# Optimization experiments

Measured on AMD Instinct MI355X. Metric: run time of the kernel, lower is better.

The kernel has to match this reference:

```python
import jax, jax.numpy as jnp
import numpy as np

B, S, E, H = 4, 1024, 1024, 16
D = E // H          # head_dim = 64
ROT = 32            # rotary dims (first ROT channels of each head)


def _rope(x, freqs):
    # x: [B, H, S, D]; freqs: [1, 1, S, ROT]
    r = freqs.shape[-1]
    xl, xr = x[..., :r], x[..., r:]
    half = r // 2
    rot = jnp.concatenate([-xl[..., half:], xl[..., :half]], axis=-1)  # rotate_half
    xl = xl * jnp.cos(freqs) + rot * jnp.sin(freqs)
    return jnp.concatenate([xl, xr], axis=-1)


def setup_inputs() -> dict:
    key = jax.random.key(0)
    ks = jax.random.split(key, 7)
    std = 0.02
    return {
        "hidden_states": jax.random.normal(ks[0], (B, S, E), jnp.float32),
        "rotary_pos_emb": jax.random.normal(ks[1], (1, S, ROT), jnp.float32),
        "q_w": jax.random.normal(ks[2], (E, E), jnp.float32) * std,
        "k_w": jax.random.normal(ks[3], (E, E), jnp.float32) * std,
        "v_w": jax.random.normal(ks[4], (E, E), jnp.float32) * std,
        "o_w": jax.random.normal(ks[5], (E, E), jnp.float32) * std,
        "o_b": jnp.zeros((E,), jnp.float32),
    }


def reference(hidden_states, rotary_pos_emb, q_w, k_w, v_w, o_w, o_b):
    bsz, tgt_len, embed_dim = hidden_states.shape
    scale = D ** -0.5

    def shape(t):  # [B, S, E] -> [B, H, S, D]
        return t.reshape(bsz, tgt_len, H, D).transpose(0, 2, 1, 3)

    q = shape(hidden_states @ q_w.T * scale)
    k = shape(hidden_states @ k_w.T)
    v = shape(hidden_states @ v_w.T)

    freqs = rotary_pos_emb[:, None, :, :]  # [1, 1, S, ROT]
    q = _rope(q, freqs)
    k = _rope(k, freqs)
    v = _rope(v, freqs)

    attn = jnp.einsum("bhqd,bhkd->bhqk", q, k)
    causal = jnp.tril(jnp.ones((tgt_len, tgt_len), bool))
    attn = jnp.where(causal, attn, jnp.finfo(attn.dtype).min)
    attn = jax.nn.softmax(attn, axis=-1)

    out = jnp.einsum("bhqk,bhkd->bhqd", attn, v)
    out = out.transpose(0, 2, 1, 3).reshape(bsz, tgt_len, embed_dim)
    return out @ o_w.T + o_b
```

## Files before the change

### kernel.cpp

```cpp
#include <hip/hip_runtime.h>
#include <hip/hip_bf16.h>

typedef __bf16 bf16;
typedef __attribute__((ext_vector_type(2))) __bf16 bf16x2;
typedef __attribute__((ext_vector_type(4))) __bf16 bf16x4;
typedef __attribute__((ext_vector_type(8))) __bf16 bf16x8;
typedef __attribute__((ext_vector_type(4))) float f32x4;

#define NB 4
#define NS 1024
#define NE 1024
#define NH 16
#define ND 64
#define NROT 32
#define NM (NB*NS)

__device__ __forceinline__ void gload_lds16(const bf16* g, void* l) {
  __builtin_amdgcn_global_load_lds(
      (const __attribute__((address_space(1))) unsigned int*)g,
      (__attribute__((address_space(3))) unsigned int*)l,
      16, 0, 0);
}

struct PrepArgs {
  const float* w0; const float* w1; const float* w2; const float* w3;
  bf16* b0; bf16* b1; bf16* b2; bf16* b3;
  const float* hs; bf16* hb;
  const float* rot; float* ct; float* st;
};
__global__ void k_prep(PrepArgs a) {
  const int y = blockIdx.y;
  const int i = blockIdx.x * 256 + threadIdx.x;
  if (y < 4) {
    const float* s = (y == 0) ? a.w0 : (y == 1) ? a.w1 : (y == 2) ? a.w2 : a.w3;
    bf16* d = (y == 0) ? a.b0 : (y == 1) ? a.b1 : (y == 2) ? a.b2 : a.b3;
    float4 v = reinterpret_cast<const float4*>(s)[i];
    bf16x4 o = { (bf16)v.x, (bf16)v.y, (bf16)v.z, (bf16)v.w };
    *reinterpret_cast<bf16x4*>(d + (size_t)i * 4) = o;
  } else if (y < 8) {
    size_t off = (size_t)(y - 4) * (NM * NE / 16);
    float4 v = reinterpret_cast<const float4*>(a.hs)[off + i];
    bf16x4 o = { (bf16)v.x, (bf16)v.y, (bf16)v.z, (bf16)v.w };
    *reinterpret_cast<bf16x4*>(a.hb + (off + i) * 4) = o;
  } else {
    if (i < NS * NROT) {
      float v = a.rot[i];
      a.ct[i] = cosf(v);
      a.st[i] = sinf(v);
    }
  }
}

__global__ __launch_bounds__(512) void k_proj(
    const bf16* __restrict__ A, const bf16* __restrict__ Wq, const bf16* __restrict__ Wk,
    const bf16* __restrict__ Wv, bf16* __restrict__ Oq, bf16* __restrict__ Ok,
    bf16* __restrict__ vt, const float* __restrict__ ct, const float* __restrict__ st)
{
  __shared__ bf16 lA[2 * 128 * 64];
  __shared__ bf16 lW[3][2 * 128 * 64];
  const int m0 = blockIdx.x * 128, n0 = blockIdx.y * 128;
  const int tid = threadIdx.x;
  const int wave = tid >> 6, lane = tid & 63;
  const int wm = wave >> 2, wn = wave & 3;
  const int fr = lane & 15, kg = lane >> 4;
  const int lrow8 = lane >> 3, lslot = lane & 7;

  auto stageG = [&](int kt, int c, int g) {
    const bf16* src = (g == 0) ? A : (g == 1) ? Wq : (g == 2) ? Wk : Wv;
    bf16* dst = (g == 0) ? lA : lW[g - 1];
    const int base0 = (g == 0) ? m0 : n0;
#pragma unroll
    for (int i = 0; i < 2; ++i) {
      int chunk = wave * 2 + i;
      int row = (chunk << 3) + lrow8;
      int slot = lslot ^ (row & 7);
      gload_lds16(src + (size_t)(base0 + row) * NE + kt + slot * 8,
                  (char*)dst + c * 16384 + chunk * 1024);
    }
  };

#pragma unroll
  for (int g = 0; g < 4; ++g) stageG(0, 0, g);
  asm volatile("s_waitcnt vmcnt(0)\n\ts_barrier" ::: "memory");

  constexpr int NT = NE / 64;
  f32x4 aq[4][2] = {}, ak[4][2] = {}, av[2][4] = {};
  bf16x8 bq[2][2], bk[2][2], bv[2][2];

  for (int t = 0; t < NT; ++t) {
    const int c = t & 1;
    const bf16* cA = lA + c * 8192;
    const bf16* cQ = lW[0] + c * 8192;
    const bf16* cK = lW[1] + c * 8192;
    const bf16* cV = lW[2] + c * 8192;

#pragma unroll
    for (int q = 0; q < 4; ++q) {
      if (t + 1 < NT) {
        if (q == 0) { stageG((t + 1) * 64, c ^ 1, 0); stageG((t + 1) * 64, c ^ 1, 1); }
        else if (q < 3) stageG((t + 1) * 64, c ^ 1, q + 1);
      }

      if (q == 0) {
        if (t > 0) {
          if (t + 1 < NT)
            asm volatile("s_waitcnt vmcnt(4)\n\ts_barrier" ::: "memory");
          else
            asm volatile("s_waitcnt vmcnt(0)\n\ts_barrier" ::: "memory");
        }
#pragma unroll
        for (int j = 0; j < 2; ++j) {
          int rb = wn * 32 + j * 16 + fr;
          int off0 = rb * 64 + (((kg + 0) ^ (rb & 7)) << 3);
          int off1 = rb * 64 + (((kg + 4) ^ (rb & 7)) << 3);
          bq[j][0] = *reinterpret_cast<const bf16x8*>(cQ + off0);
          bq[j][1] = *reinterpret_cast<const bf16x8*>(cQ + off1);
          bk[j][0] = *reinterpret_cast<const bf16x8*>(cK + off0);
          bk[j][1] = *reinterpret_cast<const bf16x8*>(cK + off1);
          bv[j][0] = *reinterpret_cast<const bf16x8*>(cV + off0);
          bv[j][1] = *reinterpret_cast<const bf16x8*>(cV + off1);
        }
      }

      bf16x8 af[2];
      {
        int ra = wm * 64 + q * 16 + fr;
        af[0] = *reinterpret_cast<const bf16x8*>(cA + ra * 64 + (((kg + 0) ^ (ra & 7)) << 3));
        af[1] = *reinterpret_cast<const bf16x8*>(cA + ra * 64 + (((kg + 4) ^ (ra & 7)) << 3));
      }

      __builtin_amdgcn_sched_barrier(0);
      __builtin_amdgcn_s_setprio(1);
#pragma unroll
      for (int kk = 0; kk < 2; ++kk)
#pragma unroll
        for (int j = 0; j < 2; ++j) {
          aq[q][j] = __builtin_amdgcn_mfma_f32_16x16x32_bf16(af[kk], bq[j][kk], aq[q][j], 0, 0, 0);
          ak[q][j] = __builtin_amdgcn_mfma_f32_16x16x32_bf16(af[kk], bk[j][kk], ak[q][j], 0, 0, 0);
          av[j][q] = __builtin_amdgcn_mfma_f32_16x16x32_bf16(bv[j][kk], af[kk], av[j][q], 0, 0, 0);
        }
      __builtin_amdgcn_s_setprio(0);
      __builtin_amdgcn_sched_barrier(0);
    }

    asm volatile("s_waitcnt lgkmcnt(0)\n\ts_barrier" ::: "memory");
  }

  const int nb = n0 + wn * 32;
  const bool ropeHalf = ((nb & 63) == 0);
  const float qscale = 0.125f * 1.44269504f;

#pragma unroll
  for (int p = 0; p < 4; ++p)
#pragma unroll
    for (int r = 0; r < 4; ++r) {
      int gm = m0 + wm * 64 + p * 16 + kg * 4 + r;
      int s = gm & (NS - 1);
      size_t rb = (size_t)gm * NE + nb;
      float q0v = aq[p][0][r] * qscale, q1v = aq[p][1][r] * qscale;
      float k0v = ak[p][0][r],          k1v = ak[p][1][r];
      if (ropeHalf) {
        float c0 = ct[s * NROT + fr],      sn0 = st[s * NROT + fr];
        float c1 = ct[s * NROT + 16 + fr], sn1 = st[s * NROT + 16 + fr];
        Oq[rb + fr]      = (bf16)(q0v * c0 - q1v * sn0);
        Oq[rb + 16 + fr] = (bf16)(q1v * c1 + q0v * sn1);
        Ok[rb + fr]      = (bf16)(k0v * c0 - k1v * sn0);
        Ok[rb + 16 + fr] = (bf16)(k1v * c1 + k0v * sn1);
      } else {
        Oq[rb + fr]      = (bf16)q0v;
        Oq[rb + 16 + fr] = (bf16)q1v;
        Ok[rb + fr]      = (bf16)k0v;
        Ok[rb + 16 + fr] = (bf16)k1v;
      }
    }

  {
    const int b = m0 >> 10;
    const int h = nb >> 6;
    const int eb = nb & 63;
    bf16* vtb = vt + ((size_t)(b * 16 + h)) * ND * NS;
#pragma unroll
    for (int i = 0; i < 4; ++i) {
      int sl = (m0 & (NS - 1)) + wm * 64 + i * 16 + fr;
#pragma unroll
      for (int r = 0; r < 4; ++r) {
        int dbase = kg * 4 + r;
        float x0 = av[0][i][r];
        float x1 = av[1][i][r];
        if (eb == 0) {
          float c0 = ct[sl * NROT + dbase],      sn0 = st[sl * NROT + dbase];
          float c1 = ct[sl * NROT + 16 + dbase], sn1 = st[sl * NROT + 16 + dbase];
          vtb[(size_t)(dbase)      * NS + sl] = (bf16)(x0 * c0 - x1 * sn0);
          vtb[(size_t)(16 + dbase) * NS + sl] = (bf16)(x1 * c1 + x0 * sn1);
        } else {
          vtb[(size_t)(32 + dbase) * NS + sl] = (bf16)x0;
          vtb[(size_t)(48 + dbase) * NS + sl] = (bf16)x1;
        }
      }
    }
  }
}

__global__ __launch_bounds__(256) void k_gemm_o(
    const bf16* __restrict__ A, const bf16* __restrict__ W, float* __restrict__ Og,
    const float* __restrict__ bias)
{
  __shared__ bf16 lA[64 * 64];
  __shared__ bf16 lB[128 * 64];
  const int m0 = blockIdx.x * 64, n0 = blockIdx.y * 128;
  const int tid = threadIdx.x;
  const int wave = tid >> 6, lane = tid & 63;
  const int wm = wave >> 1, wn = wave & 1;
  const int fr = lane & 15, kg = lane >> 4;
  const int lrow8 = lane >> 3, lslot = lane & 7;

  f32x4 acc[2][4] = {};

  for (int kt = 0; kt < NE; kt += 64) {
#pragma unroll
    for (int i = 0; i < 2; ++i) {
      int chunk = i * 4 + wave;
      int row = (chunk << 3) + lrow8;
      int slot = lslot ^ (row & 7);
      gload_lds16(A + (size_t)(m0 + row) * NE + kt + slot * 8, (char*)lA + chunk * 1024);
    }
#pragma unroll
    for (int i = 0; i < 4; ++i) {
      int chunk = i * 4 + wave;
      int row = (chunk << 3) + lrow8;
      int slot = lslot ^ (row & 7);
      gload_lds16(W + (size_t)(n0 + row) * NE + kt + slot * 8, (char*)lB + chunk * 1024);
    }
    __syncthreads();
#pragma unroll
    for (int kk = 0; kk < 2; ++kk) {
      bf16x8 af[2], bfr[4];
#pragma unroll
      for (int i = 0; i < 2; ++i) {
        int ra = wm * 32 + i * 16 + fr;
        af[i] = *reinterpret_cast<const bf16x8*>(lA + ra * 64 + (((kg + 4 * kk) ^ (ra & 7)) << 3));
      }
#pragma unroll
      for (int j = 0; j < 4; ++j) {
        int rb = wn * 64 + j * 16 + fr;
        bfr[j] = *reinterpret_cast<const bf16x8*>(lB + rb * 64 + (((kg + 4 * kk) ^ (rb & 7)) << 3));
      }
#pragma unroll
      for (int i = 0; i < 2; ++i)
#pragma unroll
        for (int j = 0; j < 4; ++j)
          acc[i][j] = __builtin_amdgcn_mfma_f32_16x16x32_bf16(af[i], bfr[j], acc[i][j], 0, 0, 0);
    }
    __syncthreads();
  }

#pragma unroll
  for (int i = 0; i < 2; ++i)
#pragma unroll
    for (int j = 0; j < 4; ++j) {
      int gc = n0 + wn * 64 + j * 16 + fr;
      float bv = bias[gc];
#pragma unroll
      for (int r = 0; r < 4; ++r) {
        int gm = m0 + wm * 32 + i * 16 + kg * 4 + r;
        Og[(size_t)gm * NE + gc] = acc[i][j][r] + bv;
      }
    }
}

__global__ __launch_bounds__(256) void k_attn(
    const bf16* __restrict__ Q, const bf16* __restrict__ K,
    const bf16* __restrict__ VT, bf16* __restrict__ O)
{
  __shared__ bf16 lK[2][64 * 64];
  __shared__ bf16 lVT[2][64 * 64];
  __shared__ bf16 lP[4][16 * 68];
  const int tid = threadIdx.x;
  const int wave = tid >> 6, lane = tid & 63;
  const int fr = lane & 15, kg = lane >> 4;

  const int qt = 15 - (blockIdx.y >> 3);
  const int bh = blockIdx.x | ((blockIdx.y & 7) << 3);
  const int b = bh >> 4, h = bh & 15;
  const int nt = qt + 1;
  const bf16* Qb  = Q + (size_t)b * NS * NE + h * 64;
  const bf16* Kb  = K + (size_t)b * NS * NE + h * 64;
  const bf16* VTb = VT + (size_t)bh * ND * NS;
  bf16* Ob = O + (size_t)b * NS * NE + h * 64;

  const int qrow0 = qt * 64 + wave * 16;

  bf16x8 qf[2];
#pragma unroll
  for (int kk = 0; kk < 2; ++kk)
    qf[kk] = *reinterpret_cast<const bf16x8*>(
        Qb + (size_t)(qrow0 + fr) * NE + kk * 32 + kg * 8);

  const int srow = lane >> 3;
  const int sslot = (lane & 7) ^ srow;
  const int r0 = wave * 8 + srow;
  const int r1 = (wave + 4) * 8 + srow;
  const bf16* kA0 = Kb + (size_t)r0 * NE + sslot * 8;
  const bf16* kA1 = Kb + (size_t)r1 * NE + sslot * 8;
  const bf16* vA0 = VTb + (size_t)r0 * NS + sslot * 8;
  const bf16* vA1 = VTb + (size_t)r1 * NS + sslot * 8;
  char* ldsKa[2] = { (char*)lK[0] + wave * 1024, (char*)lK[1] + wave * 1024 };
  char* ldsKb[2] = { (char*)lK[0] + (wave + 4) * 1024, (char*)lK[1] + (wave + 4) * 1024 };
  char* ldsVa[2] = { (char*)lVT[0] + wave * 1024, (char*)lVT[1] + wave * 1024 };
  char* ldsVb[2] = { (char*)lVT[0] + (wave + 4) * 1024, (char*)lVT[1] + (wave + 4) * 1024 };

  float m_ = -3.0e38f, l_ = 0.f;
  f32x4 oacc[4] = {};

  gload_lds16(kA0, ldsKa[0]);
  gload_lds16(kA1, ldsKb[0]);
  gload_lds16(vA0, ldsVa[0]);
  gload_lds16(vA1, ldsVb[0]);
  __syncthreads();

  for (int t = 0; t < nt; ++t) {
    const int c = t & 1;
    if (t + 1 < nt) {
      gload_lds16(kA0 + (size_t)(t + 1) * 64 * NE, ldsKa[c ^ 1]);
      gload_lds16(kA1 + (size_t)(t + 1) * 64 * NE, ldsKb[c ^ 1]);
      gload_lds16(vA0 + (t + 1) * 64, ldsVa[c ^ 1]);
      gload_lds16(vA1 + (t + 1) * 64, ldsVb[c ^ 1]);
    }

    const bf16* lKc = lK[c];
    f32x4 sacc[4] = {};
    __builtin_amdgcn_s_setprio(1);
#pragma unroll
    for (int kk = 0; kk < 2; ++kk)
#pragma unroll
      for (int j = 0; j < 4; ++j) {
        int rc = j * 16 + fr;
        bf16x8 kf = *reinterpret_cast<const bf16x8*>(
            lKc + rc * 64 + (((kg + 4 * kk) ^ (rc & 7)) << 3));
        sacc[j] = __builtin_amdgcn_mfma_f32_16x16x32_bf16(kf, qf[kk], sacc[j], 0, 0, 0);
      }
    __builtin_amdgcn_s_setprio(0);

    if (t == qt) {
      const int ql = wave * 16 + fr;
#pragma unroll
      for (int j = 0; j < 4; ++j)
#pragma unroll
        for (int r = 0; r < 4; ++r)
          if (16 * j + 4 * kg + r > ql) sacc[j][r] = -3.0e38f;
    }

    float m4 = fmaxf(fmaxf(fmaxf(sacc[0][0], sacc[0][1]), fmaxf(sacc[0][2], sacc[0][3])),
                     fmaxf(fmaxf(sacc[1][0], sacc[1][1]), fmaxf(sacc[1][2], sacc[1][3])));
    m4 = fmaxf(m4, fmaxf(fmaxf(fmaxf(sacc[2][0], sacc[2][1]), fmaxf(sacc[2][2], sacc[2][3])),
                         fmaxf(fmaxf(sacc[3][0], sacc[3][1]), fmaxf(sacc[3][2], sacc[3][3]))));
    m4 = fmaxf(m4, __shfl_xor(m4, 16));
    m4 = fmaxf(m4, __shfl_xor(m4, 32));

    if (!__all(m4 - m_ <= 8.0f)) {
      float nm = fmaxf(m_, m4);
      float corr = exp2f(m_ - nm);
      m_ = nm;
      l_ *= corr;
#pragma unroll
      for (int r = 0; r < 4; ++r) {
        float cr = __shfl(corr, kg * 4 + r);
#pragma unroll
        for (int df = 0; df < 4; ++df) oacc[df][r] *= cr;
      }
    }

    float ps = 0.f;
#pragma unroll
    for (int j = 0; j < 4; ++j) {
      float p0 = exp2f(sacc[j][0] - m_);
      float p1 = exp2f(sacc[j][1] - m_);
      float p2 = exp2f(sacc[j][2] - m_);
      float p3 = exp2f(sacc[j][3] - m_);
      ps += (p0 + p1) + (p2 + p3);
      bf16x4 pp = { (bf16)p0, (bf16)p1, (bf16)p2, (bf16)p3 };
      *reinterpret_cast<bf16x4*>(&lP[wave][fr * 68 + j * 16 + kg * 4]) = pp;
    }
    ps += __shfl_xor(ps, 16);
    ps += __shfl_xor(ps, 32);
    l_ += ps;

    const bf16* lVc = lVT[c];
    __builtin_amdgcn_s_setprio(1);
#pragma unroll
    for (int ks = 0; ks < 2; ++ks) {
      bf16x8 pf = *reinterpret_cast<const bf16x8*>(&lP[wave][fr * 68 + ks * 32 + kg * 8]);
#pragma unroll
      for (int df = 0; df < 4; ++df) {
        int d = df * 16 + fr;
        bf16x8 vf = *reinterpret_cast<const bf16x8*>(
            lVc + d * 64 + (((kg + 4 * ks) ^ (d & 7)) << 3));
        oacc[df] = __builtin_amdgcn_mfma_f32_16x16x32_bf16(pf, vf, oacc[df], 0, 0, 0);
      }
    }
    __builtin_amdgcn_s_setprio(0);

    if (t + 1 < nt)
      asm volatile("s_waitcnt vmcnt(0)\n\ts_barrier" ::: "memory");
  }

  float linv[4];
#pragma unroll
  for (int r = 0; r < 4; ++r) linv[r] = 1.0f / __shfl(l_, kg * 4 + r);
#pragma unroll
  for (int df = 0; df < 4; ++df)
#pragma unroll
    for (int r = 0; r < 4; ++r)
      Ob[(size_t)(qrow0 + kg * 4 + r) * NE + df * 16 + fr] = (bf16)(oacc[df][r] * linv[r]);
}

extern "C" void kernel_launch(void* const* d_in, const int* in_sizes, int n_in,
                              void* d_out, int out_size, void* d_ws, size_t ws_size,
                              hipStream_t stream) {
  const float* hs  = (const float*)d_in[0];
  const float* rot = (const float*)d_in[1];
  const float* qw  = (const float*)d_in[2];
  const float* kw  = (const float*)d_in[3];
  const float* vw  = (const float*)d_in[4];
  const float* ow  = (const float*)d_in[5];
  const float* obb = (const float*)d_in[6];
  float* out = (float*)d_out;

  char* ws = (char*)d_ws;
  size_t off = 0;
  bf16* hb  = (bf16*)(ws + off); off += (size_t)NM * NE * 2;
  bf16* wqb = (bf16*)(ws + off); off += (size_t)NE * NE * 2;
  bf16* wkb = (bf16*)(ws + off); off += (size_t)NE * NE * 2;
  bf16* wvb = (bf16*)(ws + off); off += (size_t)NE * NE * 2;
  bf16* wob = (bf16*)(ws + off); off += (size_t)NE * NE * 2;
  bf16* qb  = (bf16*)(ws + off); off += (size_t)NM * NE * 2;
  bf16* kb  = (bf16*)(ws + off); off += (size_t)NM * NE * 2;
  bf16* vt  = (bf16*)(ws + off); off += (size_t)NM * NE * 2;
  float* ct = (float*)(ws + off); off += (size_t)NS * NROT * 4;
  float* st = (float*)(ws + off); off += (size_t)NS * NROT * 4;
  bf16* aob = hb;

  PrepArgs pa = { qw, kw, vw, ow, wqb, wkb, wvb, wob, hs, hb, rot, ct, st };
  k_prep<<<dim3(NE * NE / 4 / 256, 9), dim3(256), 0, stream>>>(pa);

  k_proj<<<dim3(NM / 128, NE / 128), dim3(512), 0, stream>>>(
      hb, wqb, wkb, wvb, qb, kb, vt, ct, st);

  k_attn<<<dim3(8, 128), dim3(256), 0, stream>>>(qb, kb, vt, aob);

  k_gemm_o<<<dim3(NM / 64, NE / 128), dim3(256), 0, stream>>>(aob, wob, out, obb);

  (void)in_sizes; (void)n_in; (void)out_size; (void)ws_size;
}
```

Measured before the change: 96.37 us.

## Split QKV projection tile across 16 waves with simpler per-K-step staging

The fused QKV projection kernel now launches 1024 threads (16 waves) instead of 512. Each wave computes a 32x32 sub-tile instead of 64x32, which roughly halves accumulator registers per wave. Each wave now issues one async global-to-LDS load per matrix per K-step, and the per-quarter interleaving of loads with MFMAs is replaced by a single wait and barrier at the top of each K tile. More resident waves should hide latency better. The cost is more LDS fragment reads per MFMA, since weight fragments are re-read by more row groups, and less explicit overlap between loads and compute.

```diff
diff --git a/kernel.cpp b/kernel.cpp
--- a/kernel.cpp
+++ b/kernel.cpp
@@ -51,7 +51,7 @@
   }
 }
 
-__global__ __launch_bounds__(512) void k_proj(
+__global__ __launch_bounds__(1024) void k_proj(
     const bf16* __restrict__ A, const bf16* __restrict__ Wq, const bf16* __restrict__ Wk,
     const bf16* __restrict__ Wv, bf16* __restrict__ Oq, bf16* __restrict__ Ok,
     bf16* __restrict__ vt, const float* __restrict__ ct, const float* __restrict__ st)
@@ -65,82 +65,64 @@
   const int fr = lane & 15, kg = lane >> 4;
   const int lrow8 = lane >> 3, lslot = lane & 7;
 
-  auto stageG = [&](int kt, int c, int g) {
-    const bf16* src = (g == 0) ? A : (g == 1) ? Wq : (g == 2) ? Wk : Wv;
-    bf16* dst = (g == 0) ? lA : lW[g - 1];
-    const int base0 = (g == 0) ? m0 : n0;
-#pragma unroll
-    for (int i = 0; i < 2; ++i) {
-      int chunk = wave * 2 + i;
-      int row = (chunk << 3) + lrow8;
-      int slot = lslot ^ (row & 7);
-      gload_lds16(src + (size_t)(base0 + row) * NE + kt + slot * 8,
-                  (char*)dst + c * 16384 + chunk * 1024);
-    }
+  auto stage = [&](int kt, int c) {
+    const int chunk = wave;
+    const int row = (chunk << 3) + lrow8;
+    const int slot = lslot ^ (row & 7);
+    const size_t rowA = (size_t)(m0 + row) * NE + kt + slot * 8;
+    const size_t rowW = (size_t)(n0 + row) * NE + kt + slot * 8;
+    gload_lds16(A  + rowA, (char*)lA    + c * 16384 + chunk * 1024);
+    gload_lds16(Wq + rowW, (char*)lW[0] + c * 16384 + chunk * 1024);
+    gload_lds16(Wk + rowW, (char*)lW[1] + c * 16384 + chunk * 1024);
+    gload_lds16(Wv + rowW, (char*)lW[2] + c * 16384 + chunk * 1024);
   };
 
-#pragma unroll
-  for (int g = 0; g < 4; ++g) stageG(0, 0, g);
-  asm volatile("s_waitcnt vmcnt(0)\n\ts_barrier" ::: "memory");
+  stage(0, 0);
 
   constexpr int NT = NE / 64;
-  f32x4 aq[4][2] = {}, ak[4][2] = {}, av[2][4] = {};
-  bf16x8 bq[2][2], bk[2][2], bv[2][2];
+  f32x4 aq[2][2] = {}, ak[2][2] = {}, av[2][2] = {};
 
   for (int t = 0; t < NT; ++t) {
     const int c = t & 1;
+    if (t + 1 < NT) stage((t + 1) * 64, c ^ 1);
+
+    if (t + 1 < NT)
+      asm volatile("s_waitcnt vmcnt(4)\n\ts_barrier" ::: "memory");
+    else
+      asm volatile("s_waitcnt vmcnt(0)\n\ts_barrier" ::: "memory");
+
     const bf16* cA = lA + c * 8192;
     const bf16* cQ = lW[0] + c * 8192;
     const bf16* cK = lW[1] + c * 8192;
     const bf16* cV = lW[2] + c * 8192;
 
 #pragma unroll
-    for (int q = 0; q < 4; ++q) {
-      if (t + 1 < NT) {
-        if (q == 0) { stageG((t + 1) * 64, c ^ 1, 0); stageG((t + 1) * 64, c ^ 1, 1); }
-        else if (q < 3) stageG((t + 1) * 64, c ^ 1, q + 1);
-      }
-
-      if (q == 0) {
-        if (t > 0) {
-          if (t + 1 < NT)
-            asm volatile("s_waitcnt vmcnt(4)\n\ts_barrier" ::: "memory");
-          else
-            asm volatile("s_waitcnt vmcnt(0)\n\ts_barrier" ::: "memory");
-        }
+    for (int kk = 0; kk < 2; ++kk) {
+      bf16x8 af[2], bq[2], bk[2], bv[2];
+#pragma unroll
+      for (int p = 0; p < 2; ++p) {
+        int ra = wm * 32 + p * 16 + fr;
+        af[p] = *reinterpret_cast<const bf16x8*>(
+            cA + ra * 64 + (((kg + 4 * kk) ^ (ra & 7)) << 3));
+      }
+#pragma unroll
+      for (int j = 0; j < 2; ++j) {
+        int rb = wn * 32 + j * 16 + fr;
+        int off = rb * 64 + (((kg + 4 * kk) ^ (rb & 7)) << 3);
+        bq[j] = *reinterpret_cast<const bf16x8*>(cQ + off);
+        bk[j] = *reinterpret_cast<const bf16x8*>(cK + off);
+        bv[j] = *reinterpret_cast<const bf16x8*>(cV + off);
+      }
+      __builtin_amdgcn_s_setprio(1);
+#pragma unroll
+      for (int p = 0; p < 2; ++p)
 #pragma unroll
         for (int j = 0; j < 2; ++j) {
-          int rb = wn * 32 + j * 16 + fr;
-          int off0 = rb * 64 + (((kg + 0) ^ (rb & 7)) << 3);
-          int off1 = rb * 64 + (((kg + 4) ^ (rb & 7)) << 3);
-          bq[j][0] = *reinterpret_cast<const bf16x8*>(cQ + off0);
-          bq[j][1] = *reinterpret_cast<const bf16x8*>(cQ + off1);
-          bk[j][0] = *reinterpret_cast<const bf16x8*>(cK + off0);
-          bk[j][1] = *reinterpret_cast<const bf16x8*>(cK + off1);
-          bv[j][0] = *reinterpret_cast<const bf16x8*>(cV + off0);
-          bv[j][1] = *reinterpret_cast<const bf16x8*>(cV + off1);
-        }
-      }
-
-      bf16x8 af[2];
-      {
-        int ra = wm * 64 + q * 16 + fr;
-        af[0] = *reinterpret_cast<const bf16x8*>(cA + ra * 64 + (((kg + 0) ^ (ra & 7)) << 3));
-        af[1] = *reinterpret_cast<const bf16x8*>(cA + ra * 64 + (((kg + 4) ^ (ra & 7)) << 3));
-      }
-
-      __builtin_amdgcn_sched_barrier(0);
-      __builtin_amdgcn_s_setprio(1);
-#pragma unroll
-      for (int kk = 0; kk < 2; ++kk)
-#pragma unroll
-        for (int j = 0; j < 2; ++j) {
-          aq[q][j] = __builtin_amdgcn_mfma_f32_16x16x32_bf16(af[kk], bq[j][kk], aq[q][j], 0, 0, 0);
-          ak[q][j] = __builtin_amdgcn_mfma_f32_16x16x32_bf16(af[kk], bk[j][kk], ak[q][j], 0, 0, 0);
-          av[j][q] = __builtin_amdgcn_mfma_f32_16x16x32_bf16(bv[j][kk], af[kk], av[j][q], 0, 0, 0);
+          aq[p][j] = __builtin_amdgcn_mfma_f32_16x16x32_bf16(af[p], bq[j], aq[p][j], 0, 0, 0);
+          ak[p][j] = __builtin_amdgcn_mfma_f32_16x16x32_bf16(af[p], bk[j], ak[p][j], 0, 0, 0);
+          av[j][p] = __builtin_amdgcn_mfma_f32_16x16x32_bf16(bv[j], af[p], av[j][p], 0, 0, 0);
         }
       __builtin_amdgcn_s_setprio(0);
-      __builtin_amdgcn_sched_barrier(0);
     }
 
     asm volatile("s_waitcnt lgkmcnt(0)\n\ts_barrier" ::: "memory");
@@ -151,10 +133,10 @@
   const float qscale = 0.125f * 1.44269504f;
 
 #pragma unroll
-  for (int p = 0; p < 4; ++p)
+  for (int p = 0; p < 2; ++p)
 #pragma unroll
     for (int r = 0; r < 4; ++r) {
-      int gm = m0 + wm * 64 + p * 16 + kg * 4 + r;
+      int gm = m0 + wm * 32 + p * 16 + kg * 4 + r;
       int s = gm & (NS - 1);
       size_t rb = (size_t)gm * NE + nb;
       float q0v = aq[p][0][r] * qscale, q1v = aq[p][1][r] * qscale;
@@ -180,13 +162,13 @@
     const int eb = nb & 63;
     bf16* vtb = vt + ((size_t)(b * 16 + h)) * ND * NS;
 #pragma unroll
-    for (int i = 0; i < 4; ++i) {
-      int sl = (m0 & (NS - 1)) + wm * 64 + i * 16 + fr;
+    for (int p = 0; p < 2; ++p) {
+      int sl = (m0 & (NS - 1)) + wm * 32 + p * 16 + fr;
 #pragma unroll
       for (int r = 0; r < 4; ++r) {
         int dbase = kg * 4 + r;
-        float x0 = av[0][i][r];
-        float x1 = av[1][i][r];
+        float x0 = av[0][p][r];
+        float x1 = av[1][p][r];
         if (eb == 0) {
           float c0 = ct[sl * NROT + dbase],      sn0 = st[sl * NROT + dbase];
           float c1 = ct[sl * NROT + 16 + dbase], sn1 = st[sl * NROT + 16 + dbase];
@@ -443,7 +425,7 @@
   PrepArgs pa = { qw, kw, vw, ow, wqb, wkb, wvb, wob, hs, hb, rot, ct, st };
   k_prep<<<dim3(NE * NE / 4 / 256, 9), dim3(256), 0, stream>>>(pa);
 
-  k_proj<<<dim3(NM / 128, NE / 128), dim3(512), 0, stream>>>(
+  k_proj<<<dim3(NM / 128, NE / 128), dim3(1024), 0, stream>>>(
       hb, wqb, wkb, wvb, qb, kb, vt, ct, st);
 
   k_attn<<<dim3(8, 128), dim3(256), 0, stream>>>(qb, kb, vt, aob);
```

Result: faster. 93.17 us, median of 3 (-3.3%).
